# Kernel tuning notes

Hardware: AMD Instinct MI355X
Metric: run time of the kernel (lower is better)

Reference implementation:

```python
import jax, jax.numpy as jnp
import numpy as np

N_EMBD = 768
HEAD_SIZE = 64

def setup_inputs() -> dict:
    key = jax.random.key(0)
    ks = jax.random.split(key, 9)
    B, S = 8, 2048
    scale = 1.0 / np.sqrt(N_EMBD)
    return {
        "q": jax.random.normal(ks[0], (B, S, N_EMBD), jnp.float32),
        "k": jax.random.normal(ks[1], (B, S, N_EMBD), jnp.float32),
        "v": jax.random.normal(ks[2], (B, S, N_EMBD), jnp.float32),
        "Wq": jax.random.normal(ks[3], (N_EMBD, HEAD_SIZE), jnp.float32) * scale,
        "bq": jnp.zeros((HEAD_SIZE,), jnp.float32),
        "Wk": jax.random.normal(ks[4], (N_EMBD, HEAD_SIZE), jnp.float32) * scale,
        "bk": jnp.zeros((HEAD_SIZE,), jnp.float32),
        "Wv": jax.random.normal(ks[5], (N_EMBD, HEAD_SIZE), jnp.float32) * scale,
        "bv": jnp.zeros((HEAD_SIZE,), jnp.float32),
    }

def reference(q, k, v, Wq, bq, Wk, bk, Wv, bv):
    # NOTE: original scales by sqrt(C) where C = n_embd (input dim), not head_size.
    C = q.shape[-1]
    qi = q @ Wq + bq  # [B,S,H]
    ki = k @ Wk + bk
    vi = v @ Wv + bv
    att = jnp.einsum('bsh,bth->bst', qi, ki) / jnp.sqrt(jnp.float32(C))
    att = jax.nn.softmax(att, axis=-1)
    out = jnp.einsum('bst,bth->bsh', att, vi)
    return out
```

## Files before the change

### kernel.cpp

```cpp
#include <hip/hip_runtime.h>

#define Bn 8
#define Sn 2048
#define Cn 768
#define Hn 64
#define BS (Bn * Sn)

typedef __attribute__((ext_vector_type(8))) short bf16x8;
typedef __attribute__((ext_vector_type(4))) float f32x4;

__device__ __forceinline__ unsigned short f2bf(float x) {
  unsigned int u = __builtin_bit_cast(unsigned int, x);
  u += 0x7FFFu + ((u >> 16) & 1u);
  return (unsigned short)(u >> 16);
}

__global__ __launch_bounds__(256) void wconv(const float* __restrict__ Wq,
                                             const float* __restrict__ Wk,
                                             const float* __restrict__ Wv,
                                             unsigned short* __restrict__ Wt) {
  int idx = blockIdx.x * 256 + threadIdx.x;
  int mat = idx / (Cn * Hn);
  int rem = idx - mat * (Cn * Hn);
  int c = rem / Hn, h = rem - c * Hn;
  const float* W = (mat == 0) ? Wq : (mat == 1) ? Wk : Wv;
  Wt[mat * (Hn * Cn) + h * Cn + c] = f2bf(W[rem]);
}

__global__ __launch_bounds__(256) void proj(const float* __restrict__ q,
                                            const float* __restrict__ k,
                                            const float* __restrict__ v,
                                            const float* __restrict__ bq,
                                            const float* __restrict__ bk,
                                            const float* __restrict__ bv,
                                            const unsigned short* __restrict__ Wt,
                                            unsigned short* __restrict__ qi,
                                            unsigned short* __restrict__ ki,
                                            unsigned short* __restrict__ vi) {
  const int mat  = blockIdx.x >> 8;
  const int row0 = (blockIdx.x & 255) * 64;
  const float* X    = (mat == 0) ? q  : (mat == 1) ? k  : v;
  const float* bias = (mat == 0) ? bq : (mat == 1) ? bk : bv;
  unsigned short* Y = (mat == 0) ? qi : (mat == 1) ? ki : vi;
  const unsigned short* Wm = Wt + mat * (Hn * Cn);
  const float scale = (mat == 0) ? 0.03608439182435161f : 1.0f;

  __shared__ __align__(16) unsigned char Xs[64 * 128];
  __shared__ __align__(16) unsigned char Ws[64 * 128];

  const int tid  = threadIdx.x;
  const int lane = tid & 63;
  const int w    = tid >> 6;
  const int col  = lane & 15;
  const int grp  = lane >> 4;

  f32x4 acc[4] = {};

  for (int kc = 0; kc < 12; ++kc) {
    __syncthreads();
#pragma unroll
    for (int i = 0; i < 4; ++i) {
      int f4 = tid + i * 256;
      int r  = f4 >> 4;
      int c4 = f4 & 15;
      float4 xv = *(const float4*)(X + (size_t)(row0 + r) * Cn + kc * 64 + c4 * 4);
      ushort4 hv;
      hv.x = f2bf(xv.x); hv.y = f2bf(xv.y); hv.z = f2bf(xv.z); hv.w = f2bf(xv.w);
      *(ushort4*)(Xs + r * 128 + ((c4 * 8) ^ ((r & 7) << 4))) = hv;
    }
    {
      int r = tid >> 2;
      int p = tid & 3;
      const uint4* src = (const uint4*)(Wm + (size_t)r * Cn + kc * 64);
      uint4 a  = src[p * 2];
      uint4 b2 = src[p * 2 + 1];
      *(uint4*)(Ws + r * 128 + ((p * 32) ^ ((r & 7) << 4)))        = a;
      *(uint4*)(Ws + r * 128 + (((p * 32) + 16) ^ ((r & 7) << 4))) = b2;
    }
    __syncthreads();
    const int rloc = w * 16 + col;
#pragma unroll
    for (int ks = 0; ks < 2; ++ks) {
      bf16x8 a = *(const bf16x8*)(Xs + rloc * 128 + ((ks * 64 + grp * 16) ^ ((rloc & 7) << 4)));
#pragma unroll
      for (int nf = 0; nf < 4; ++nf) {
        int wr = nf * 16 + col;
        bf16x8 bfr = *(const bf16x8*)(Ws + wr * 128 + ((ks * 64 + grp * 16) ^ ((wr & 7) << 4)));
        acc[nf] = __builtin_amdgcn_mfma_f32_16x16x32_bf16(a, bfr, acc[nf], 0, 0, 0);
      }
    }
  }
#pragma unroll
  for (int nf = 0; nf < 4; ++nf) {
    int h = nf * 16 + col;
    float bv = bias[h];
#pragma unroll
    for (int r2 = 0; r2 < 4; ++r2) {
      int row = row0 + w * 16 + grp * 4 + r2;
      Y[(size_t)row * Hn + h] = f2bf((acc[nf][r2] + bv) * scale);
    }
  }
}

template <int SPLIT>
__global__ __launch_bounds__(256) void attn(const unsigned short* __restrict__ qi,
                                            const unsigned short* __restrict__ ki,
                                            const unsigned short* __restrict__ vi,
                                            float* __restrict__ pacc,
                                            float* __restrict__ pm,
                                            float* __restrict__ pl,
                                            float* __restrict__ out,
                                            int tpb) {
  const int bq    = blockIdx.x & 255;
  const int split = blockIdx.x >> 8;
  const int b  = bq >> 5;
  const int s0 = (bq & 31) * 64;
  const int t0 = split * tpb;
  const unsigned short* Qb = qi + ((size_t)b * Sn + s0) * Hn;
  const unsigned short* Kb = ki + (size_t)b * Sn * Hn;
  const unsigned short* Vb = vi + (size_t)b * Sn * Hn;

  __shared__ __align__(16) unsigned char Ks[64 * 128];
  __shared__ __align__(16) unsigned char Vt[64 * 128];
  __shared__ __align__(16) unsigned char Ps[4 * 16 * 128];

  const int tid  = threadIdx.x;
  const int lane = tid & 63;
  const int w    = tid >> 6;
  const int col  = lane & 15;
  const int grp  = lane >> 4;

  bf16x8 qa[2];
#pragma unroll
  for (int ks2 = 0; ks2 < 2; ++ks2)
    qa[ks2] = *(const bf16x8*)(Qb + (size_t)(w * 16 + col) * Hn + ks2 * 32 + grp * 8);

  f32x4 acc[4] = {};
  float m[4], l[4];
#pragma unroll
  for (int r = 0; r < 4; ++r) { m[r] = -1e30f; l[r] = 0.0f; }

  for (int t = t0; t < t0 + tpb; ++t) {
    const unsigned short* Kt = Kb + t * 64 * Hn;
    const unsigned short* Vg = Vb + t * 64 * Hn;
    __syncthreads();
    {
      int kr = tid >> 2, p = tid & 3;
      const uint4* src = (const uint4*)(Kt + kr * Hn);
      uint4 a  = src[p * 2];
      uint4 b2 = src[p * 2 + 1];
      *(uint4*)(Ks + kr * 128 + ((p * 32) ^ ((kr & 7) << 4)))        = a;
      *(uint4*)(Ks + kr * 128 + (((p * 32) + 16) ^ ((kr & 7) << 4))) = b2;
    }
    {
      int kp = tid >> 3;
      int dg = tid & 7;
      uint4 v0 = *(const uint4*)(Vg + (2 * kp) * Hn + dg * 8);
      uint4 v1 = *(const uint4*)(Vg + (2 * kp + 1) * Hn + dg * 8);
      const unsigned short* a0 = (const unsigned short*)&v0;
      const unsigned short* a1 = (const unsigned short*)&v1;
#pragma unroll
      for (int j0 = 0; j0 < 8; ++j0) {
        int j = (j0 + dg) & 7;
        int d = dg * 8 + j;
        unsigned int pk = (unsigned int)a0[j] | ((unsigned int)a1[j] << 16);
        *(unsigned int*)(Vt + d * 128 + ((4 * kp) ^ ((d & 7) << 4))) = pk;
      }
    }
    __syncthreads();
    f32x4 sf[4] = {};
#pragma unroll
    for (int ks2 = 0; ks2 < 2; ++ks2) {
#pragma unroll
      for (int nf = 0; nf < 4; ++nf) {
        int kr = nf * 16 + col;
        bf16x8 bfr = *(const bf16x8*)(Ks + kr * 128 + ((ks2 * 64 + grp * 16) ^ ((kr & 7) << 4)));
        sf[nf] = __builtin_amdgcn_mfma_f32_16x16x32_bf16(qa[ks2], bfr, sf[nf], 0, 0, 0);
      }
    }
    float mn[4], fs[4];
#pragma unroll
    for (int r = 0; r < 4; ++r) {
      float mx = fmaxf(fmaxf(sf[0][r], sf[1][r]), fmaxf(sf[2][r], sf[3][r]));
#pragma unroll
      for (int off = 1; off < 16; off <<= 1)
        mx = fmaxf(mx, __shfl_xor(mx, off, 64));
      mn[r] = fmaxf(m[r], mx);
      fs[r] = __expf(m[r] - mn[r]);
      m[r]  = mn[r];
    }
#pragma unroll
    for (int nf = 0; nf < 4; ++nf)
#pragma unroll
      for (int r = 0; r < 4; ++r)
        sf[nf][r] = __expf(sf[nf][r] - mn[r]);
#pragma unroll
    for (int r = 0; r < 4; ++r) {
      float sm = sf[0][r] + sf[1][r] + sf[2][r] + sf[3][r];
#pragma unroll
      for (int off = 1; off < 16; off <<= 1)
        sm += __shfl_xor(sm, off, 64);
      l[r] = l[r] * fs[r] + sm;
    }
#pragma unroll
    for (int nf = 0; nf < 4; ++nf) {
#pragma unroll
      for (int r = 0; r < 4; ++r) {
        acc[nf][r] *= fs[r];
        int prow = grp * 4 + r;
        int key  = nf * 16 + col;
        *(unsigned short*)(Ps + w * 2048 + prow * 128 + ((key * 2) ^ ((prow & 7) << 4))) =
            f2bf(sf[nf][r]);
      }
    }
#pragma unroll
    for (int kk = 0; kk < 2; ++kk) {
      bf16x8 pa = *(const bf16x8*)(Ps + w * 2048 + col * 128 +
                                   ((kk * 64 + grp * 16) ^ ((col & 7) << 4)));
#pragma unroll
      for (int nf = 0; nf < 4; ++nf) {
        int dr = nf * 16 + col;
        bf16x8 bv = *(const bf16x8*)(Vt + dr * 128 + ((kk * 64 + grp * 16) ^ ((dr & 7) << 4)));
        acc[nf] = __builtin_amdgcn_mfma_f32_16x16x32_bf16(pa, bv, acc[nf], 0, 0, 0);
      }
    }
  }
  if (SPLIT) {
    const size_t sb = (size_t)split * BS + (size_t)b * Sn;
#pragma unroll
    for (int nf = 0; nf < 4; ++nf) {
#pragma unroll
      for (int r = 0; r < 4; ++r) {
        int row = s0 + w * 16 + grp * 4 + r;
        pacc[(sb + row) * Hn + nf * 16 + col] = acc[nf][r];
      }
    }
    if (col == 0) {
#pragma unroll
      for (int r = 0; r < 4; ++r) {
        int row = s0 + w * 16 + grp * 4 + r;
        pm[sb + row] = m[r];
        pl[sb + row] = l[r];
      }
    }
  } else {
#pragma unroll
    for (int nf = 0; nf < 4; ++nf) {
#pragma unroll
      for (int r = 0; r < 4; ++r) {
        int row = s0 + w * 16 + grp * 4 + r;
        out[((size_t)b * Sn + row) * Hn + nf * 16 + col] = acc[nf][r] / l[r];
      }
    }
  }
}

__global__ __launch_bounds__(256) void combine(const float* __restrict__ pacc,
                                               const float* __restrict__ pm,
                                               const float* __restrict__ pl,
                                               float* __restrict__ out,
                                               int nsplit) {
  int gid = blockIdx.x * 256 + threadIdx.x;
  int gr  = gid >> 4;
  int dq  = (gid & 15) * 4;
  float M = -1e30f;
  for (int s = 0; s < nsplit; ++s) M = fmaxf(M, pm[(size_t)s * BS + gr]);
  float L = 0.0f;
  float4 o = make_float4(0.f, 0.f, 0.f, 0.f);
  for (int s = 0; s < nsplit; ++s) {
    float wgt = __expf(pm[(size_t)s * BS + gr] - M);
    L += pl[(size_t)s * BS + gr] * wgt;
    float4 p = *(const float4*)(pacc + ((size_t)s * BS + gr) * Hn + dq);
    o.x += p.x * wgt; o.y += p.y * wgt; o.z += p.z * wgt; o.w += p.w * wgt;
  }
  float inv = 1.0f / L;
  float4 r = make_float4(o.x * inv, o.y * inv, o.z * inv, o.w * inv);
  *(float4*)(out + (size_t)gr * Hn + dq) = r;
}

extern "C" void kernel_launch(void* const* d_in, const int* in_sizes, int n_in,
                              void* d_out, int out_size, void* d_ws, size_t ws_size,
                              hipStream_t stream) {
  const float* q  = (const float*)d_in[0];
  const float* k  = (const float*)d_in[1];
  const float* v  = (const float*)d_in[2];
  const float* Wq = (const float*)d_in[3];
  const float* bq = (const float*)d_in[4];
  const float* Wk = (const float*)d_in[5];
  const float* bk = (const float*)d_in[6];
  const float* Wv = (const float*)d_in[7];
  const float* bv = (const float*)d_in[8];
  float* out = (float*)d_out;

  unsigned short* Wt = (unsigned short*)d_ws;
  unsigned short* qi = Wt + 3 * Hn * Cn;
  unsigned short* ki = qi + (size_t)BS * Hn;
  unsigned short* vi = ki + (size_t)BS * Hn;
  float* pacc = (float*)(vi + (size_t)BS * Hn);

  const size_t base_bytes = (size_t)(3 * Hn * Cn + 3 * (size_t)BS * Hn) * 2;
  int nsplit = 4;
  while (nsplit > 1 &&
         base_bytes + (size_t)nsplit * ((size_t)BS * Hn * 4 + 2 * (size_t)BS * 4) > ws_size)
    nsplit >>= 1;
  bool direct = (base_bytes + (size_t)nsplit * ((size_t)BS * Hn * 4 + 2 * (size_t)BS * 4) > ws_size);

  float* pm = pacc + (size_t)nsplit * BS * Hn;
  float* pl = pm + (size_t)nsplit * BS;

  wconv<<<dim3((3 * Cn * Hn) / 256), dim3(256), 0, stream>>>(Wq, Wk, Wv, Wt);
  proj<<<dim3(768), dim3(256), 0, stream>>>(q, k, v, bq, bk, bv, Wt, qi, ki, vi);
  if (direct) {
    attn<0><<<dim3(256), dim3(256), 0, stream>>>(qi, ki, vi, nullptr, nullptr, nullptr, out, 32);
  } else {
    attn<1><<<dim3(256 * nsplit), dim3(256), 0, stream>>>(qi, ki, vi, pacc, pm, pl, nullptr,
                                                          32 / nsplit);
    combine<<<dim3(BS * 16 / 256), dim3(256), 0, stream>>>(pacc, pm, pl, out, nsplit);
  }
}
```

Measured before the change: 87.75 us.

## Load X fragments directly to registers and double-buffer W tiles in projection

```diff
diff --git a/kernel.cpp b/kernel.cpp
--- a/kernel.cpp
+++ b/kernel.cpp
@@ -45,8 +45,7 @@
   const unsigned short* Wm = Wt + mat * (Hn * Cn);
   const float scale = (mat == 0) ? 0.03608439182435161f : 1.0f;
 
-  __shared__ __align__(16) unsigned char Xs[64 * 128];
-  __shared__ __align__(16) unsigned char Ws[64 * 128];
+  __shared__ __align__(16) unsigned char Wbuf[2][64 * 128];
 
   const int tid  = threadIdx.x;
   const int lane = tid & 63;
@@ -54,42 +53,64 @@
   const int col  = lane & 15;
   const int grp  = lane >> 4;
 
+  const float* Xrow = X + (size_t)(row0 + w * 16 + col) * Cn + grp * 8;
+  const int wr_ = tid >> 2;
+  const int wp_ = tid & 3;
+  const unsigned short* Wrow = Wm + (size_t)wr_ * Cn + wp_ * 16;
+  const int wo0 = wr_ * 128 + ((wp_ * 32) ^ ((wr_ & 7) << 4));
+  const int wo1 = wr_ * 128 + (((wp_ * 32) + 16) ^ ((wr_ & 7) << 4));
+
+  float4 acur[4], anext[4];
+  uint4 wra, wrb;
+#pragma unroll
+  for (int ks = 0; ks < 2; ++ks) {
+    acur[ks * 2]     = *(const float4*)(Xrow + ks * 32);
+    acur[ks * 2 + 1] = *(const float4*)(Xrow + ks * 32 + 4);
+  }
+  wra = *(const uint4*)(Wrow);
+  wrb = *(const uint4*)(Wrow + 8);
+  *(uint4*)(Wbuf[0] + wo0) = wra;
+  *(uint4*)(Wbuf[0] + wo1) = wrb;
+  __syncthreads();
+
   f32x4 acc[4] = {};
 
-  for (int kc = 0; kc < 12; ++kc) {
-    __syncthreads();
-#pragma unroll
-    for (int i = 0; i < 4; ++i) {
-      int f4 = tid + i * 256;
-      int r  = f4 >> 4;
-      int c4 = f4 & 15;
-      float4 xv = *(const float4*)(X + (size_t)(row0 + r) * Cn + kc * 64 + c4 * 4);
-      ushort4 hv;
-      hv.x = f2bf(xv.x); hv.y = f2bf(xv.y); hv.z = f2bf(xv.z); hv.w = f2bf(xv.w);
-      *(ushort4*)(Xs + r * 128 + ((c4 * 8) ^ ((r & 7) << 4))) = hv;
-    }
-    {
-      int r = tid >> 2;
-      int p = tid & 3;
-      const uint4* src = (const uint4*)(Wm + (size_t)r * Cn + kc * 64);
-      uint4 a  = src[p * 2];
-      uint4 b2 = src[p * 2 + 1];
-      *(uint4*)(Ws + r * 128 + ((p * 32) ^ ((r & 7) << 4)))        = a;
-      *(uint4*)(Ws + r * 128 + (((p * 32) + 16) ^ ((r & 7) << 4))) = b2;
-    }
-    __syncthreads();
-    const int rloc = w * 16 + col;
+  for (int c = 0; c < 12; ++c) {
+    if (c < 11) {
+#pragma unroll
+      for (int ks = 0; ks < 2; ++ks) {
+        anext[ks * 2]     = *(const float4*)(Xrow + (c + 1) * 64 + ks * 32);
+        anext[ks * 2 + 1] = *(const float4*)(Xrow + (c + 1) * 64 + ks * 32 + 4);
+      }
+      wra = *(const uint4*)(Wrow + (c + 1) * 64);
+      wrb = *(const uint4*)(Wrow + (c + 1) * 64 + 8);
+    }
+    const unsigned char* Wb = Wbuf[c & 1];
 #pragma unroll
     for (int ks = 0; ks < 2; ++ks) {
-      bf16x8 a = *(const bf16x8*)(Xs + rloc * 128 + ((ks * 64 + grp * 16) ^ ((rloc & 7) << 4)));
+      const float4 p0 = acur[ks * 2], p1 = acur[ks * 2 + 1];
+      bf16x8 a;
+      a[0] = (short)f2bf(p0.x); a[1] = (short)f2bf(p0.y);
+      a[2] = (short)f2bf(p0.z); a[3] = (short)f2bf(p0.w);
+      a[4] = (short)f2bf(p1.x); a[5] = (short)f2bf(p1.y);
+      a[6] = (short)f2bf(p1.z); a[7] = (short)f2bf(p1.w);
 #pragma unroll
       for (int nf = 0; nf < 4; ++nf) {
-        int wr = nf * 16 + col;
-        bf16x8 bfr = *(const bf16x8*)(Ws + wr * 128 + ((ks * 64 + grp * 16) ^ ((wr & 7) << 4)));
+        int wc = nf * 16 + col;
+        bf16x8 bfr = *(const bf16x8*)(Wb + wc * 128 + ((ks * 64 + grp * 16) ^ ((wc & 7) << 4)));
         acc[nf] = __builtin_amdgcn_mfma_f32_16x16x32_bf16(a, bfr, acc[nf], 0, 0, 0);
       }
     }
-  }
+    if (c < 11) {
+      unsigned char* Wn = Wbuf[(c + 1) & 1];
+      *(uint4*)(Wn + wo0) = wra;
+      *(uint4*)(Wn + wo1) = wrb;
+#pragma unroll
+      for (int i = 0; i < 4; ++i) acur[i] = anext[i];
+      __syncthreads();
+    }
+  }
+
 #pragma unroll
   for (int nf = 0; nf < 4; ++nf) {
     int h = nf * 16 + col;
```

After: 86.83 us. Within noise of the previous version (-1.0%).

## Rewrite projection as LDS-free single-wave blocks with register double-buffered loads

Applied to the files above, without the earlier changes.

```diff
diff --git a/kernel.cpp b/kernel.cpp
--- a/kernel.cpp
+++ b/kernel.cpp
@@ -27,77 +27,96 @@
   Wt[mat * (Hn * Cn) + h * Cn + c] = f2bf(W[rem]);
 }
 
-__global__ __launch_bounds__(256) void proj(const float* __restrict__ q,
-                                            const float* __restrict__ k,
-                                            const float* __restrict__ v,
-                                            const float* __restrict__ bq,
-                                            const float* __restrict__ bk,
-                                            const float* __restrict__ bv,
-                                            const unsigned short* __restrict__ Wt,
-                                            unsigned short* __restrict__ qi,
-                                            unsigned short* __restrict__ ki,
-                                            unsigned short* __restrict__ vi) {
-  const int mat  = blockIdx.x >> 8;
-  const int row0 = (blockIdx.x & 255) * 64;
+__global__ __launch_bounds__(64, 3) void proj(const float* __restrict__ q,
+                                              const float* __restrict__ k,
+                                              const float* __restrict__ v,
+                                              const float* __restrict__ bq,
+                                              const float* __restrict__ bk,
+                                              const float* __restrict__ bv,
+                                              const unsigned short* __restrict__ Wt,
+                                              unsigned short* __restrict__ qi,
+                                              unsigned short* __restrict__ ki,
+                                              unsigned short* __restrict__ vi) {
+  const int bid  = blockIdx.x;
+  const int mat  = bid >> 10;
+  const int row0 = (bid & 1023) * 16;
   const float* X    = (mat == 0) ? q  : (mat == 1) ? k  : v;
   const float* bias = (mat == 0) ? bq : (mat == 1) ? bk : bv;
   unsigned short* Y = (mat == 0) ? qi : (mat == 1) ? ki : vi;
   const unsigned short* Wm = Wt + mat * (Hn * Cn);
   const float scale = (mat == 0) ? 0.03608439182435161f : 1.0f;
 
-  __shared__ __align__(16) unsigned char Xs[64 * 128];
-  __shared__ __align__(16) unsigned char Ws[64 * 128];
-
-  const int tid  = threadIdx.x;
-  const int lane = tid & 63;
-  const int w    = tid >> 6;
+  const int lane = threadIdx.x & 63;
   const int col  = lane & 15;
   const int grp  = lane >> 4;
 
+  const float* Xrow = X + (size_t)(row0 + col) * Cn + grp * 8;
+
+  const unsigned short* Wl = Wm + (size_t)col * Cn + grp * 8;
+
+  float4 ax[2][2][2];
+  bf16x8 bw[2][8];
+
+#pragma unroll
+  for (int d = 0; d < 2; ++d) {
+#pragma unroll
+    for (int ks = 0; ks < 2; ++ks) {
+      ax[d][ks][0] = *(const float4*)(Xrow + d * 64 + ks * 32);
+      ax[d][ks][1] = *(const float4*)(Xrow + d * 64 + ks * 32 + 4);
+    }
+#pragma unroll
+    for (int nf = 0; nf < 4; ++nf)
+#pragma unroll
+      for (int ks = 0; ks < 2; ++ks)
+        bw[d][nf * 2 + ks] =
+            *(const bf16x8*)(Wl + (size_t)(nf * 16) * Cn + d * 64 + ks * 32);
+  }
+
   f32x4 acc[4] = {};
 
-  for (int kc = 0; kc < 12; ++kc) {
-    __syncthreads();
-#pragma unroll
-    for (int i = 0; i < 4; ++i) {
-      int f4 = tid + i * 256;
-      int r  = f4 >> 4;
-      int c4 = f4 & 15;
-      float4 xv = *(const float4*)(X + (size_t)(row0 + r) * Cn + kc * 64 + c4 * 4);
-      ushort4 hv;
-      hv.x = f2bf(xv.x); hv.y = f2bf(xv.y); hv.z = f2bf(xv.z); hv.w = f2bf(xv.w);
-      *(ushort4*)(Xs + r * 128 + ((c4 * 8) ^ ((r & 7) << 4))) = hv;
-    }
-    {
-      int r = tid >> 2;
-      int p = tid & 3;
-      const uint4* src = (const uint4*)(Wm + (size_t)r * Cn + kc * 64);
-      uint4 a  = src[p * 2];
-      uint4 b2 = src[p * 2 + 1];
-      *(uint4*)(Ws + r * 128 + ((p * 32) ^ ((r & 7) << 4)))        = a;
-      *(uint4*)(Ws + r * 128 + (((p * 32) + 16) ^ ((r & 7) << 4))) = b2;
-    }
-    __syncthreads();
-    const int rloc = w * 16 + col;
+#pragma unroll
+  for (int c = 0; c < 12; ++c) {
+    const int buf = c & 1;
+    bf16x8 av[2];
 #pragma unroll
     for (int ks = 0; ks < 2; ++ks) {
-      bf16x8 a = *(const bf16x8*)(Xs + rloc * 128 + ((ks * 64 + grp * 16) ^ ((rloc & 7) << 4)));
-#pragma unroll
-      for (int nf = 0; nf < 4; ++nf) {
-        int wr = nf * 16 + col;
-        bf16x8 bfr = *(const bf16x8*)(Ws + wr * 128 + ((ks * 64 + grp * 16) ^ ((wr & 7) << 4)));
-        acc[nf] = __builtin_amdgcn_mfma_f32_16x16x32_bf16(a, bfr, acc[nf], 0, 0, 0);
-      }
-    }
-  }
+      const float4 p0 = ax[buf][ks][0], p1 = ax[buf][ks][1];
+      av[ks][0] = (short)f2bf(p0.x); av[ks][1] = (short)f2bf(p0.y);
+      av[ks][2] = (short)f2bf(p0.z); av[ks][3] = (short)f2bf(p0.w);
+      av[ks][4] = (short)f2bf(p1.x); av[ks][5] = (short)f2bf(p1.y);
+      av[ks][6] = (short)f2bf(p1.z); av[ks][7] = (short)f2bf(p1.w);
+    }
+    bf16x8 bv0[8];
+#pragma unroll
+    for (int i = 0; i < 8; ++i) bv0[i] = bw[buf][i];
+    if (c < 10) {
+#pragma unroll
+      for (int ks = 0; ks < 2; ++ks) {
+        ax[buf][ks][0] = *(const float4*)(Xrow + (c + 2) * 64 + ks * 32);
+        ax[buf][ks][1] = *(const float4*)(Xrow + (c + 2) * 64 + ks * 32 + 4);
+      }
+#pragma unroll
+      for (int nf = 0; nf < 4; ++nf)
+#pragma unroll
+        for (int ks = 0; ks < 2; ++ks)
+          bw[buf][nf * 2 + ks] =
+              *(const bf16x8*)(Wl + (size_t)(nf * 16) * Cn + (c + 2) * 64 + ks * 32);
+    }
+#pragma unroll
+    for (int ks = 0; ks < 2; ++ks)
+#pragma unroll
+      for (int nf = 0; nf < 4; ++nf)
+        acc[nf] = __builtin_amdgcn_mfma_f32_16x16x32_bf16(av[ks], bv0[nf * 2 + ks], acc[nf], 0, 0, 0);
+  }
+
 #pragma unroll
   for (int nf = 0; nf < 4; ++nf) {
     int h = nf * 16 + col;
-    float bv = bias[h];
+    float bb = bias[h];
 #pragma unroll
     for (int r2 = 0; r2 < 4; ++r2) {
-      int row = row0 + w * 16 + grp * 4 + r2;
-      Y[(size_t)row * Hn + h] = f2bf((acc[nf][r2] + bv) * scale);
+      int row = row0 + grp * 4 + r2;
+      Y[(size_t)row * Hn + h] = f2bf((acc[nf][r2] + bb) * scale);
     }
   }
 }
@@ -309,7 +328,7 @@
   float* pl = pm + (size_t)nsplit * BS;
 
   wconv<<<dim3((3 * Cn * Hn) / 256), dim3(256), 0, stream>>>(Wq, Wk, Wv, Wt);
-  proj<<<dim3(768), dim3(256), 0, stream>>>(q, k, v, bq, bk, bv, Wt, qi, ki, vi);
+  proj<<<dim3(3 * 1024), dim3(64), 0, stream>>>(q, k, v, bq, bk, bv, Wt, qi, ki, vi);
   if (direct) {
     attn<0><<<dim3(256), dim3(256), 0, stream>>>(qi, ki, vi, nullptr, nullptr, nullptr, out, 32);
   } else {
```

Result: slower. 112.5 us (+28.2%).

## Split projection GEMM along K into two partial passes plus a reduce kernel

Applied to the files above, without the earlier changes.

```diff
diff --git a/kernel.cpp b/kernel.cpp
--- a/kernel.cpp
+++ b/kernel.cpp
@@ -30,20 +30,19 @@
 __global__ __launch_bounds__(256) void proj(const float* __restrict__ q,
                                             const float* __restrict__ k,
                                             const float* __restrict__ v,
-                                            const float* __restrict__ bq,
-                                            const float* __restrict__ bk,
-                                            const float* __restrict__ bv,
                                             const unsigned short* __restrict__ Wt,
-                                            unsigned short* __restrict__ qi,
-                                            unsigned short* __restrict__ ki,
-                                            unsigned short* __restrict__ vi) {
-  const int mat  = blockIdx.x >> 8;
-  const int row0 = (blockIdx.x & 255) * 64;
-  const float* X    = (mat == 0) ? q  : (mat == 1) ? k  : v;
-  const float* bias = (mat == 0) ? bq : (mat == 1) ? bk : bv;
-  unsigned short* Y = (mat == 0) ? qi : (mat == 1) ? ki : vi;
+                                            float* __restrict__ part,
+                                            int psplit) {
+  const int per_mat = psplit << 8;
+  const int mat = blockIdx.x / per_mat;
+  const int rem = blockIdx.x - mat * per_mat;
+  const int sp  = rem >> 8;
+  const int row0 = (rem & 255) * 64;
+  const int kb     = sp * (Cn / 2) * (psplit - 1);
+  const int nchunk = (Cn / 64) / psplit;
+  const float* X = (mat == 0) ? q : (mat == 1) ? k : v;
   const unsigned short* Wm = Wt + mat * (Hn * Cn);
-  const float scale = (mat == 0) ? 0.03608439182435161f : 1.0f;
+  float* P = part + ((size_t)(sp * 3 + mat) * BS + row0) * Hn;
 
   __shared__ __align__(16) unsigned char Xs[64 * 128];
   __shared__ __align__(16) unsigned char Ws[64 * 128];
@@ -56,14 +55,15 @@
 
   f32x4 acc[4] = {};
 
-  for (int kc = 0; kc < 12; ++kc) {
+  for (int c = 0; c < nchunk; ++c) {
+    const int k0 = kb + c * 64;
     __syncthreads();
 #pragma unroll
     for (int i = 0; i < 4; ++i) {
       int f4 = tid + i * 256;
       int r  = f4 >> 4;
       int c4 = f4 & 15;
-      float4 xv = *(const float4*)(X + (size_t)(row0 + r) * Cn + kc * 64 + c4 * 4);
+      float4 xv = *(const float4*)(X + (size_t)(row0 + r) * Cn + k0 + c4 * 4);
       ushort4 hv;
       hv.x = f2bf(xv.x); hv.y = f2bf(xv.y); hv.z = f2bf(xv.z); hv.w = f2bf(xv.w);
       *(ushort4*)(Xs + r * 128 + ((c4 * 8) ^ ((r & 7) << 4))) = hv;
@@ -71,7 +71,7 @@
     {
       int r = tid >> 2;
       int p = tid & 3;
-      const uint4* src = (const uint4*)(Wm + (size_t)r * Cn + kc * 64);
+      const uint4* src = (const uint4*)(Wm + (size_t)r * Cn + k0);
       uint4 a  = src[p * 2];
       uint4 b2 = src[p * 2 + 1];
       *(uint4*)(Ws + r * 128 + ((p * 32) ^ ((r & 7) << 4)))        = a;
@@ -93,13 +93,42 @@
 #pragma unroll
   for (int nf = 0; nf < 4; ++nf) {
     int h = nf * 16 + col;
-    float bv = bias[h];
 #pragma unroll
     for (int r2 = 0; r2 < 4; ++r2) {
-      int row = row0 + w * 16 + grp * 4 + r2;
-      Y[(size_t)row * Hn + h] = f2bf((acc[nf][r2] + bv) * scale);
-    }
-  }
+      int row = w * 16 + grp * 4 + r2;
+      P[(size_t)row * Hn + h] = acc[nf][r2];
+    }
+  }
+}
+
+__global__ __launch_bounds__(256) void preduce(const float* __restrict__ part,
+                                               const float* __restrict__ bq,
+                                               const float* __restrict__ bk,
+                                               const float* __restrict__ bv,
+                                               unsigned short* __restrict__ qi,
+                                               unsigned short* __restrict__ ki,
+                                               unsigned short* __restrict__ vi,
+                                               int psplit) {
+  int gid = blockIdx.x * 256 + threadIdx.x;
+  int mat = gid / (BS * 16);
+  int rem = gid - mat * (BS * 16);
+  int row = rem >> 4;
+  int dq  = (rem & 15) * 4;
+  float4 s = *(const float4*)(part + ((size_t)mat * BS + row) * Hn + dq);
+  if (psplit == 2) {
+    float4 t = *(const float4*)(part + ((size_t)(3 + mat) * BS + row) * Hn + dq);
+    s.x += t.x; s.y += t.y; s.z += t.z; s.w += t.w;
+  }
+  const float* bias = (mat == 0) ? bq : (mat == 1) ? bk : bv;
+  unsigned short* Y = (mat == 0) ? qi : (mat == 1) ? ki : vi;
+  float4 bb = *(const float4*)(bias + dq);
+  float sc = (mat == 0) ? 0.03608439182435161f : 1.0f;
+  ushort4 o;
+  o.x = f2bf((s.x + bb.x) * sc);
+  o.y = f2bf((s.y + bb.y) * sc);
+  o.z = f2bf((s.z + bb.z) * sc);
+  o.w = f2bf((s.w + bb.w) * sc);
+  *(ushort4*)(Y + (size_t)row * Hn + dq) = o;
 }
 
 template <int SPLIT>
@@ -296,20 +325,29 @@
   unsigned short* qi = Wt + 3 * Hn * Cn;
   unsigned short* ki = qi + (size_t)BS * Hn;
   unsigned short* vi = ki + (size_t)BS * Hn;
-  float* pacc = (float*)(vi + (size_t)BS * Hn);
+  float* shared_f = (float*)(vi + (size_t)BS * Hn);
 
   const size_t base_bytes = (size_t)(3 * Hn * Cn + 3 * (size_t)BS * Hn) * 2;
+  const size_t avail = (ws_size > base_bytes) ? ws_size - base_bytes : 0;
+
+  const size_t proj_part_bytes = (size_t)3 * BS * Hn * 4;
+  int psplit = (avail >= 2 * proj_part_bytes) ? 2 : 1;
+
   int nsplit = 4;
   while (nsplit > 1 &&
-         base_bytes + (size_t)nsplit * ((size_t)BS * Hn * 4 + 2 * (size_t)BS * 4) > ws_size)
+         (size_t)nsplit * ((size_t)BS * Hn * 4 + 2 * (size_t)BS * 4) > avail)
     nsplit >>= 1;
-  bool direct = (base_bytes + (size_t)nsplit * ((size_t)BS * Hn * 4 + 2 * (size_t)BS * 4) > ws_size);
-
-  float* pm = pacc + (size_t)nsplit * BS * Hn;
-  float* pl = pm + (size_t)nsplit * BS;
+  bool direct = ((size_t)nsplit * ((size_t)BS * Hn * 4 + 2 * (size_t)BS * 4) > avail);
+
+  float* ppart = shared_f;
+  float* pacc  = shared_f;
+  float* pm    = pacc + (size_t)nsplit * BS * Hn;
+  float* pl    = pm + (size_t)nsplit * BS;
 
   wconv<<<dim3((3 * Cn * Hn) / 256), dim3(256), 0, stream>>>(Wq, Wk, Wv, Wt);
-  proj<<<dim3(768), dim3(256), 0, stream>>>(q, k, v, bq, bk, bv, Wt, qi, ki, vi);
+  proj<<<dim3(3 * psplit * 256), dim3(256), 0, stream>>>(q, k, v, Wt, ppart, psplit);
+  preduce<<<dim3(3 * BS * 16 / 256), dim3(256), 0, stream>>>(ppart, bq, bk, bv, qi, ki, vi,
+                                                             psplit);
   if (direct) {
     attn<0><<<dim3(256), dim3(256), 0, stream>>>(qi, ki, vi, nullptr, nullptr, nullptr, out, 32);
   } else {
```

After: 96.12 us. +9.5%, slower.
